# Performance work log

Measured on AMD Instinct MI355X. Metric: run time of the kernel, lower is better.

Reference implementation:

```python
import jax, jax.numpy as jnp
import numpy as np

NEG_SLOPE = 0.01  # torch nn.LeakyReLU default
B, C, H, W = 2, 128, 192, 192
K = 4            # num_cls
O = 12 * 5       # out_channels = 12 * num_mix


def _lrelu(x):
    return jnp.where(x >= 0, x, NEG_SLOPE * x)


def _conv1x1(x, w, b):
    # x: [B,K,C,H,W] (or [B,C,H,W] broadcast via K in w), w: [K,O,C], b: [K,O]
    y = jnp.einsum('bkchw,koc->bkohw', x, w)
    return y + b[None, :, :, None, None]


def setup_inputs() -> dict:
    key = jax.random.key(0)
    ks = jax.random.split(key, 12)
    s = 1.0 / np.sqrt(C)
    inp = {
        'fusion_context': jax.random.normal(ks[0], (B, C, H, W), jnp.float32),
        'seg': jax.random.randint(ks[1], (B, 1, H, W), 0, K, jnp.int64),
        'W1':  jax.random.normal(ks[2], (K, C, C), jnp.float32) * s,
        'b1':  jax.random.normal(ks[3], (K, C), jnp.float32) * s,
        'Wr1': jax.random.normal(ks[4], (K, C, C), jnp.float32) * s,
        'br1': jax.random.normal(ks[5], (K, C), jnp.float32) * s,
        'Wr2': jax.random.normal(ks[6], (K, C, C), jnp.float32) * s,
        'br2': jax.random.normal(ks[7], (K, C), jnp.float32) * s,
        'W3':  jax.random.normal(ks[8], (K, C, C), jnp.float32) * s,
        'b3':  jax.random.normal(ks[9], (K, C), jnp.float32) * s,
        'W4':  jax.random.normal(ks[10], (K, O, C), jnp.float32) * s,
        'b4':  jax.random.normal(ks[11], (K, O), jnp.float32) * s,
    }
    return inp


def reference(fusion_context, seg, W1, b1, Wr1, br1, Wr2, br2, W3, b3, W4, b4):
    x = fusion_context[:, None]                      # [B,1,C,H,W] -> broadcast over K towers
    x = jnp.broadcast_to(x, (B, K, C, H, W))
    h = _conv1x1(x, W1, b1)                          # conv1x1(ep_ch, ep_ch)
    # ResBlock_1x1: x + conv(lrelu(conv(x)))
    r = _conv1x1(_lrelu(_conv1x1(h, Wr1, br1)), Wr2, br2)
    h = h + r
    h = _conv1x1(h, W3, b3)                          # conv1x1(ep_ch, ep_ch)
    h = _lrelu(h)                                    # LeakyReLU
    conv_outs = _conv1x1(h, W4, b4)                  # [B,K,O,H,W]
    # one-hot mask-and-sum over classes
    seg2 = seg[:, 0]                                 # [B,H,W]
    one_hot = jax.nn.one_hot(seg2, K, dtype=conv_outs.dtype)  # [B,H,W,K]
    one_hot = jnp.transpose(one_hot, (0, 3, 1, 2))   # [B,K,H,W]
    out = jnp.sum(conv_outs * one_hot[:, :, None], axis=1)    # [B,O,H,W]
    return out
```

## Files before the change

### kernel.cpp

```cpp
#include <hip/hip_runtime.h>
#include <hip/hip_bf16.h>
#include <cstdint>
#include <cstddef>

constexpr int kB = 2, kC = 128, kH = 192, kW = 192, kK = 4, kO = 60;
constexpr int kHW  = kH * kW;
constexpr int NPIX = kB * kHW;
constexpr int P    = 96;
constexpr int WPB  = kHW / P;
constexpr int NWIN = NPIX / P;
constexpr int MAXG = 9;
constexpr float kSlope = 0.01f;

constexpr size_t WB_OFF    = 0;
constexpr size_t WB4_OFF   = 524288;
constexpr size_t BIAS_OFF  = 589824;
constexpr size_t BIAS4_OFF = 598016;
constexpr size_t WS_NEED   = 599040;

typedef __attribute__((ext_vector_type(8))) short bf16x8;
typedef __attribute__((ext_vector_type(4))) float f32x4;

__device__ __forceinline__ unsigned short f2bf(float f) {
  unsigned u = __float_as_uint(f);
  u += 0x7FFF + ((u >> 16) & 1);
  return (unsigned short)(u >> 16);
}
__device__ __forceinline__ float bf2f(unsigned short u) {
  return __uint_as_float(((unsigned)u) << 16);
}
__device__ __forceinline__ float load1(const float* p) { return *p; }
__device__ __forceinline__ float load1(const __hip_bfloat16* p) {
  return bf2f(*reinterpret_cast<const unsigned short*>(p));
}
__device__ __forceinline__ bf16x8 load_wfrag(const __hip_bfloat16* p) {
  return *reinterpret_cast<const bf16x8*>(p);
}
__device__ __forceinline__ bf16x8 load_wfrag(const float* p) {
  bf16x8 r;
#pragma unroll
  for (int j = 0; j < 8; ++j) r[j] = (short)f2bf(p[j]);
  return r;
}

__device__ __forceinline__ int xgrp(int r, int g) {
  return (g + r + (r >> 3)) & 15;
}

struct alignas(16) Smem {
  unsigned short Xs[P][kC];
  unsigned short Ys[P][kC];
  short ord[MAXG * 16];
  unsigned char kg[MAXG + 3];
  int cnt[kK], gpre[kK + 1], first[kK];
  int s_f32, s_onz;
};

template<typename T>
__device__ __forceinline__ void prep_body(
    const T* W1, const T* Wr1, const T* Wr2, const T* W3, const T* W4,
    const T* b1, const T* br1, const T* br2, const T* b3, const T* b4,
    char* ws, int gid) {
  unsigned short* WB  = (unsigned short*)(ws + WB_OFF);
  unsigned short* WB4 = (unsigned short*)(ws + WB4_OFF);
  float* BS  = (float*)(ws + BIAS_OFF);
  float* BS4 = (float*)(ws + BIAS4_OFF);
  if (gid < 32768) {
    const int lk = gid >> 11, fl = gid & 2047, f = fl >> 6, lane = fl & 63;
    const int l = lk >> 2, k = lk & 3;
    const int rb = f >> 3, oi = (f >> 2) & 1, ks = f & 3;
    const int quad = lane >> 4, col = lane & 15;
    const int row = rb * 32 + oi * 16 + col, c0 = ks * 32 + quad * 8;
    const T* Wsrc = (l == 0) ? W1 : (l == 1) ? Wr1 : (l == 2) ? Wr2 : W3;
    bf16x8 v = load_wfrag(Wsrc + ((size_t)(k * kC + row)) * kC + c0);
    *reinterpret_cast<bf16x8*>(WB + (size_t)lk * 16384 + f * 512 + lane * 8) = v;
  } else if (gid < 36864) {
    const int g2 = gid - 32768, k = g2 >> 10, fl = g2 & 1023, f = fl >> 6, lane = fl & 63;
    const int rb = f >> 2, ks = f & 3, quad = lane >> 4, col = lane & 15;
    const int row = rb * 16 + col, c0 = ks * 32 + quad * 8;
    bf16x8 v;
    if (row < kO) v = load_wfrag(W4 + ((size_t)(k * kO + row)) * kC + c0);
    else { for (int j = 0; j < 8; ++j) v[j] = 0; }
    *reinterpret_cast<bf16x8*>(WB4 + (size_t)k * 8192 + f * 512 + lane * 8) = v;
  } else if (gid < 38912) {
    const int g2 = gid - 36864, l = g2 >> 9, kn = g2 & 511, k = kn >> 7, n = kn & 127;
    const T* bsrc = (l == 0) ? b1 : (l == 1) ? br1 : (l == 2) ? br2 : b3;
    BS[g2] = load1(bsrc + k * kC + n);
  } else if (gid < 39168) {
    const int g2 = gid - 38912, k = g2 >> 6, n = g2 & 63;
    BS4[g2] = (n < kO) ? load1(b4 + k * kO + n) : 0.f;
  }
}

__global__ __launch_bounds__(256) void prep_kernel(
    const void* W1, const void* Wr1, const void* Wr2, const void* W3, const void* W4,
    const void* b1, const void* br1, const void* br2, const void* b3, const void* b4,
    char* ws) {
  __shared__ int s_f32;
  if (threadIdx.x == 0) s_f32 = 0;
  __syncthreads();
  const unsigned short h = ((const unsigned short*)W1)[threadIdx.x];
  if (((h >> 7) & 0xFF) >= 0x84) atomicAdd(&s_f32, 1);
  __syncthreads();
  const int gid = blockIdx.x * 256 + threadIdx.x;
  if (s_f32 > 8)
    prep_body<float>((const float*)W1, (const float*)Wr1, (const float*)Wr2,
                     (const float*)W3, (const float*)W4, (const float*)b1,
                     (const float*)br1, (const float*)br2, (const float*)b3,
                     (const float*)b4, ws, gid);
  else
    prep_body<__hip_bfloat16>((const __hip_bfloat16*)W1, (const __hip_bfloat16*)Wr1,
                              (const __hip_bfloat16*)Wr2, (const __hip_bfloat16*)W3,
                              (const __hip_bfloat16*)W4, (const __hip_bfloat16*)b1,
                              (const __hip_bfloat16*)br1, (const __hip_bfloat16*)br2,
                              (const __hip_bfloat16*)b3, (const __hip_bfloat16*)b4,
                              ws, gid);
}

template<bool SNIFFX>
__device__ __forceinline__ void prologue(const void* xraw, const void* segraw,
                                         Smem& sm, int bb, int hw0, int tid) {
  if (tid == 0) { sm.s_f32 = 0; sm.s_onz = 0; }
  if (tid < kK) sm.cnt[tid] = 0;
  __syncthreads();
  if constexpr (SNIFFX) {
    const unsigned short h = ((const unsigned short*)xraw)[tid];
    if (((h >> 7) & 0xFF) >= 0x84) atomicAdd(&sm.s_f32, 1);
  }
  if (tid < 288 && (tid & 1) && ((const unsigned*)segraw)[tid] != 0)
    atomicAdd(&sm.s_onz, 1);
  __syncthreads();
  const bool is64 = (sm.s_onz < 4);
  int myk = 0, myidx = 0;
  if (tid < P) {
    const int pg = bb * kHW + hw0 + tid;
    myk = is64 ? (int)((const long long*)segraw)[pg]
               : ((const int*)segraw)[pg];
    myidx = atomicAdd(&sm.cnt[myk], 1);
    if (myidx == 0) sm.first[myk] = tid;
  }
  __syncthreads();
  if (tid == 0) {
    int g = 0;
    for (int k = 0; k < kK; ++k) {
      sm.gpre[k] = g;
      const int gc = (sm.cnt[k] + 15) >> 4;
      for (int j = 0; j < gc; ++j) sm.kg[g + j] = (unsigned char)k;
      g += gc;
    }
    sm.gpre[kK] = g;
  }
  __syncthreads();
  if (tid < P) sm.ord[sm.gpre[myk] * 16 + myidx] = (short)tid;
  const int ngrp = sm.gpre[kK];
  if (tid < ngrp * 16) {
    const int g = tid >> 4, k2 = sm.kg[g];
    const int rel = tid - sm.gpre[k2] * 16;
    if (rel >= sm.cnt[k2])
      sm.ord[tid] = (short)(sm.first[k2] | 256);
  }
}

template<typename T>
__device__ __forceinline__ void stage(const void* xraw, unsigned short (*Xs)[kC],
                                      int bb, int hw0, int tid) {
  const T* x = (const T*)xraw;
  const size_t base = (size_t)bb * kC * kHW + hw0;
  if constexpr (sizeof(T) == 4) {
#pragma unroll
    for (int it = 0; it < 6; ++it) {
      const int flat = it * 512 + tid;
      const int c = flat / 24, j = flat - c * 24;
      const float4 v = *reinterpret_cast<const float4*>(
          (const float*)x + base + (size_t)c * kHW + j * 4);
      const float vv[4] = {v.x, v.y, v.z, v.w};
#pragma unroll
      for (int jj = 0; jj < 4; ++jj) {
        const int r = j * 4 + jj;
        Xs[r][xgrp(r, c >> 3) * 8 + (c & 7)] = f2bf(vv[jj]);
      }
    }
  } else {
#pragma unroll
    for (int it = 0; it < 3; ++it) {
      const int flat = it * 512 + tid;
      const int c = flat / 12, j = flat - c * 12;
      const bf16x8 v = *reinterpret_cast<const bf16x8*>(
          (const unsigned short*)x + base + (size_t)c * kHW + j * 8);
#pragma unroll
      for (int jj = 0; jj < 8; ++jj) {
        const int r = j * 8 + jj;
        Xs[r][xgrp(r, c >> 3) * 8 + (c & 7)] = (unsigned short)v[jj];
      }
    }
  }
}

template<typename T>
__device__ __forceinline__ void output(void* outraw, const float* Obuf,
                                       int bb, int hw0, int tid) {
  T* ob = (T*)outraw + (size_t)bb * kO * kHW + hw0;
  if constexpr (sizeof(T) == 4) {
#pragma unroll
    for (int it = 0; it < 3; ++it) {
      const int t = it * 512 + tid;
      if (t < 1440) {
        const int o = t / 24, q = t - o * 24;
        float4 v;
        v.x = Obuf[(q * 4 + 0) * 61 + o];
        v.y = Obuf[(q * 4 + 1) * 61 + o];
        v.z = Obuf[(q * 4 + 2) * 61 + o];
        v.w = Obuf[(q * 4 + 3) * 61 + o];
        *reinterpret_cast<float4*>((float*)ob + (size_t)o * kHW + q * 4) = v;
      }
    }
  } else {
#pragma unroll
    for (int it = 0; it < 6; ++it) {
      const int t = it * 512 + tid;
      if (t < 2880) {
        const int o = t / 48, q = t - o * 48;
        const unsigned u = (unsigned)f2bf(Obuf[(q * 2) * 61 + o]) |
                           ((unsigned)f2bf(Obuf[(q * 2 + 1) * 61 + o]) << 16);
        *reinterpret_cast<unsigned*>((unsigned short*)ob + (size_t)o * kHW + q * 2) = u;
      }
    }
  }
}

template<bool LRELU, bool RES>
__device__ __forceinline__ void layerP(const unsigned short (*src)[kC],
                                       unsigned short (*dst)[kC],
                                       const unsigned short* __restrict__ WBl,
                                       const float* __restrict__ BSl,
                                       const Smem& sm, int tid) {
  const int wave = tid >> 6, lane = tid & 63, quad = lane >> 4, col = lane & 15;
  const int rb = wave & 3, ch2 = wave >> 2;
  const int gs = sm.gpre[ch2 * 2], ge = sm.gpre[ch2 * 2 + 2];
  int curk = -1;
  bf16x8 a[2][4];
  float bs[2][4];
  for (int g = gs; g < ge; ++g) {
    const int k = sm.kg[g];
    if (k != curk) {
      curk = k;
      const unsigned short* wk = WBl + (size_t)k * 16384 + lane * 8;
#pragma unroll
      for (int oi = 0; oi < 2; ++oi) {
#pragma unroll
        for (int ks = 0; ks < 4; ++ks)
          a[oi][ks] = *reinterpret_cast<const bf16x8*>(wk + (((rb * 2 + oi) * 4 + ks) << 9));
        const float4 bv = *reinterpret_cast<const float4*>(
            BSl + k * kC + rb * 32 + oi * 16 + quad * 4);
        bs[oi][0] = bv.x; bs[oi][1] = bv.y; bs[oi][2] = bv.z; bs[oi][3] = bv.w;
      }
    }
    const int ov  = sm.ord[g * 16 + col];
    const int row = ov & 255;
    bf16x8 bfr[4];
#pragma unroll
    for (int ks = 0; ks < 4; ++ks)
      bfr[ks] = *reinterpret_cast<const bf16x8*>(&src[row][xgrp(row, ks * 4 + quad) * 8]);
#pragma unroll
    for (int oi = 0; oi < 2; ++oi) {
      f32x4 acc = {0.f, 0.f, 0.f, 0.f};
#pragma unroll
      for (int ks = 0; ks < 4; ++ks)
        acc = __builtin_amdgcn_mfma_f32_16x16x32_bf16(a[oi][ks], bfr[ks], acc, 0, 0, 0);
      if (ov < 256) {
        const int nb = rb * 32 + oi * 16 + quad * 4;
        unsigned short* dp = &dst[row][xgrp(row, nb >> 3) * 8 + (nb & 7)];
        float v[4];
#pragma unroll
        for (int r = 0; r < 4; ++r) {
          float t = acc[r] + bs[oi][r];
          if constexpr (LRELU) t = (t >= 0.f) ? t : kSlope * t;
          v[r] = t;
        }
        if constexpr (RES) {
          const short4 rv = *reinterpret_cast<const short4*>(dp);
          v[0] += bf2f((unsigned short)rv.x);
          v[1] += bf2f((unsigned short)rv.y);
          v[2] += bf2f((unsigned short)rv.z);
          v[3] += bf2f((unsigned short)rv.w);
        }
        short4 pk;
        pk.x = (short)f2bf(v[0]); pk.y = (short)f2bf(v[1]);
        pk.z = (short)f2bf(v[2]); pk.w = (short)f2bf(v[3]);
        *reinterpret_cast<short4*>(dp) = pk;
      }
    }
  }
}

__device__ __forceinline__ void layer5P(const unsigned short (*src)[kC],
                                        float* __restrict__ Obuf,
                                        const unsigned short* __restrict__ WB4,
                                        const float* __restrict__ BS4,
                                        const Smem& sm, int tid) {
  const int wave = tid >> 6, lane = tid & 63, quad = lane >> 4, col = lane & 15;
  const int rb = wave & 3, ch2 = wave >> 2;
  const int gs = sm.gpre[ch2 * 2], ge = sm.gpre[ch2 * 2 + 2];
  int curk = -1;
  bf16x8 a[4];
  float bs[4];
  for (int g = gs; g < ge; ++g) {
    const int k = sm.kg[g];
    if (k != curk) {
      curk = k;
      const unsigned short* wk = WB4 + (size_t)k * 8192 + lane * 8;
#pragma unroll
      for (int ks = 0; ks < 4; ++ks)
        a[ks] = *reinterpret_cast<const bf16x8*>(wk + ((rb * 4 + ks) << 9));
      const float4 bv = *reinterpret_cast<const float4*>(BS4 + k * 64 + rb * 16 + quad * 4);
      bs[0] = bv.x; bs[1] = bv.y; bs[2] = bv.z; bs[3] = bv.w;
    }
    const int ov  = sm.ord[g * 16 + col];
    const int row = ov & 255;
    bf16x8 bfr[4];
#pragma unroll
    for (int ks = 0; ks < 4; ++ks)
      bfr[ks] = *reinterpret_cast<const bf16x8*>(&src[row][xgrp(row, ks * 4 + quad) * 8]);
    f32x4 acc = {0.f, 0.f, 0.f, 0.f};
#pragma unroll
    for (int ks = 0; ks < 4; ++ks)
      acc = __builtin_amdgcn_mfma_f32_16x16x32_bf16(a[ks], bfr[ks], acc, 0, 0, 0);
    if (ov < 256) {
#pragma unroll
      for (int r = 0; r < 4; ++r) {
        const int n = rb * 16 + quad * 4 + r;
        if (n < kO) Obuf[row * 61 + n] = acc[r] + bs[r];
      }
    }
  }
}

__global__ __launch_bounds__(512) void fused_main(const void* xraw, const void* segraw,
                                                  void* outraw,
                                                  const char* __restrict__ ws) {
  __shared__ Smem sm;
  const int tid = threadIdx.x, wi = blockIdx.x;
  const int bb = wi / WPB, hw0 = (wi - bb * WPB) * P;
  prologue<true>(xraw, segraw, sm, bb, hw0, tid);
  const bool isf32 = (sm.s_f32 > 16);
  if (isf32) stage<float>(xraw, sm.Xs, bb, hw0, tid);
  else       stage<__hip_bfloat16>(xraw, sm.Xs, bb, hw0, tid);
  __syncthreads();

  const unsigned short* WB  = (const unsigned short*)(ws + WB_OFF);
  const unsigned short* WB4 = (const unsigned short*)(ws + WB4_OFF);
  const float* BS  = (const float*)(ws + BIAS_OFF);
  const float* BS4 = (const float*)(ws + BIAS4_OFF);

  layerP<false, false>(sm.Xs, sm.Ys, WB,              BS,        sm, tid); __syncthreads();
  layerP<true,  false>(sm.Ys, sm.Xs, WB + 4 * 16384,  BS + 512,  sm, tid); __syncthreads();
  layerP<false, true >(sm.Xs, sm.Ys, WB + 8 * 16384,  BS + 1024, sm, tid); __syncthreads();
  layerP<true,  false>(sm.Ys, sm.Xs, WB + 12 * 16384, BS + 1536, sm, tid); __syncthreads();
  float* Obuf = (float*)sm.Ys;
  layer5P(sm.Xs, Obuf, WB4, BS4, sm, tid);     __syncthreads();

  if (isf32) output<float>(outraw, Obuf, bb, hw0, tid);
  else       output<__hip_bfloat16>(outraw, Obuf, bb, hw0, tid);
}

template<typename T, bool LRELU, bool RES>
__device__ __forceinline__ void layerF(const unsigned short (*src)[kC],
                                       unsigned short (*dst)[kC],
                                       const T* __restrict__ W,
                                       const T* __restrict__ bia,
                                       const Smem& sm, int tid) {
  const int wave = tid >> 6, lane = tid & 63, quad = lane >> 4, col = lane & 15;
  const int rb = wave & 3, ch2 = wave >> 2;
  const int gs = sm.gpre[ch2 * 2], ge = sm.gpre[ch2 * 2 + 2];
  int curk = -1;
  bf16x8 a[2][4];
  float bs[2][4];
  for (int g = gs; g < ge; ++g) {
    const int k = sm.kg[g];
    if (k != curk) {
      curk = k;
      const T* Wk = W + (size_t)k * kC * kC;
      const T* bk = bia + (size_t)k * kC;
#pragma unroll
      for (int oi = 0; oi < 2; ++oi) {
        const int ra = rb * 32 + oi * 16 + col;
#pragma unroll
        for (int ks = 0; ks < 4; ++ks)
          a[oi][ks] = load_wfrag(Wk + (size_t)ra * kC + ks * 32 + quad * 8);
#pragma unroll
        for (int r = 0; r < 4; ++r)
          bs[oi][r] = load1(bk + rb * 32 + oi * 16 + quad * 4 + r);
      }
    }
    const int ov  = sm.ord[g * 16 + col];
    const int row = ov & 255;
    bf16x8 bfr[4];
#pragma unroll
    for (int ks = 0; ks < 4; ++ks)
      bfr[ks] = *reinterpret_cast<const bf16x8*>(&src[row][xgrp(row, ks * 4 + quad) * 8]);
#pragma unroll
    for (int oi = 0; oi < 2; ++oi) {
      f32x4 acc = {0.f, 0.f, 0.f, 0.f};
#pragma unroll
      for (int ks = 0; ks < 4; ++ks)
        acc = __builtin_amdgcn_mfma_f32_16x16x32_bf16(a[oi][ks], bfr[ks], acc, 0, 0, 0);
      if (ov < 256) {
        const int nb = rb * 32 + oi * 16 + quad * 4;
        unsigned short* dp = &dst[row][xgrp(row, nb >> 3) * 8 + (nb & 7)];
        float v[4];
#pragma unroll
        for (int r = 0; r < 4; ++r) {
          float t = acc[r] + bs[oi][r];
          if constexpr (LRELU) t = (t >= 0.f) ? t : kSlope * t;
          v[r] = t;
        }
        if constexpr (RES) {
          const short4 rv = *reinterpret_cast<const short4*>(dp);
          v[0] += bf2f((unsigned short)rv.x);
          v[1] += bf2f((unsigned short)rv.y);
          v[2] += bf2f((unsigned short)rv.z);
          v[3] += bf2f((unsigned short)rv.w);
        }
        short4 pk;
        pk.x = (short)f2bf(v[0]); pk.y = (short)f2bf(v[1]);
        pk.z = (short)f2bf(v[2]); pk.w = (short)f2bf(v[3]);
        *reinterpret_cast<short4*>(dp) = pk;
      }
    }
  }
}

template<typename T>
__device__ __forceinline__ void layer5F(const unsigned short (*src)[kC],
                                        float* __restrict__ Obuf,
                                        const T* __restrict__ W4,
                                        const T* __restrict__ b4,
                                        const Smem& sm, int tid) {
  const int wave = tid >> 6, lane = tid & 63, quad = lane >> 4, col = lane & 15;
  const int rb = wave & 3, ch2 = wave >> 2;
  const int gs = sm.gpre[ch2 * 2], ge = sm.gpre[ch2 * 2 + 2];
  int curk = -1;
  bf16x8 a[4];
  float bs[4];
  for (int g = gs; g < ge; ++g) {
    const int k = sm.kg[g];
    if (k != curk) {
      curk = k;
      const T* Wk = W4 + (size_t)k * kO * kC;
      const T* bk = b4 + (size_t)k * kO;
      const int ra = min(rb * 16 + col, kO - 1);
#pragma unroll
      for (int ks = 0; ks < 4; ++ks)
        a[ks] = load_wfrag(Wk + (size_t)ra * kC + ks * 32 + quad * 8);
#pragma unroll
      for (int r = 0; r < 4; ++r) {
        const int n = rb * 16 + quad * 4 + r;
        bs[r] = (n < kO) ? load1(bk + n) : 0.f;
      }
    }
    const int ov  = sm.ord[g * 16 + col];
    const int row = ov & 255;
    bf16x8 bfr[4];
#pragma unroll
    for (int ks = 0; ks < 4; ++ks)
      bfr[ks] = *reinterpret_cast<const bf16x8*>(&src[row][xgrp(row, ks * 4 + quad) * 8]);
    f32x4 acc = {0.f, 0.f, 0.f, 0.f};
#pragma unroll
    for (int ks = 0; ks < 4; ++ks)
      acc = __builtin_amdgcn_mfma_f32_16x16x32_bf16(a[ks], bfr[ks], acc, 0, 0, 0);
    if (ov < 256) {
#pragma unroll
      for (int r = 0; r < 4; ++r) {
        const int n = rb * 16 + quad * 4 + r;
        if (n < kO) Obuf[row * 61 + n] = acc[r] + bs[r];
      }
    }
  }
}

template<typename T>
__device__ __forceinline__ void run_fall(
    const void* xraw, void* outraw,
    const void* W1, const void* b1, const void* Wr1, const void* br1,
    const void* Wr2, const void* br2, const void* W3, const void* b3,
    const void* W4, const void* b4,
    Smem& sm, int bb, int hw0, int tid) {
  stage<T>(xraw, sm.Xs, bb, hw0, tid);
  __syncthreads();
  layerF<T, false, false>(sm.Xs, sm.Ys, (const T*)W1,  (const T*)b1,  sm, tid); __syncthreads();
  layerF<T, true,  false>(sm.Ys, sm.Xs, (const T*)Wr1, (const T*)br1, sm, tid); __syncthreads();
  layerF<T, false, true >(sm.Xs, sm.Ys, (const T*)Wr2, (const T*)br2, sm, tid); __syncthreads();
  layerF<T, true,  false>(sm.Ys, sm.Xs, (const T*)W3,  (const T*)b3,  sm, tid); __syncthreads();
  float* Obuf = (float*)sm.Ys;
  layer5F<T>(sm.Xs, Obuf, (const T*)W4, (const T*)b4, sm, tid);
  __syncthreads();
  output<T>(outraw, Obuf, bb, hw0, tid);
}

__global__ __launch_bounds__(512) void fused_fallback(
    const void* xraw, const void* segraw,
    const void* W1, const void* b1, const void* Wr1, const void* br1,
    const void* Wr2, const void* br2, const void* W3, const void* b3,
    const void* W4, const void* b4, void* outraw) {
  __shared__ Smem sm;
  const int tid = threadIdx.x, wi = blockIdx.x;
  const int bb = wi / WPB, hw0 = (wi - bb * WPB) * P;
  prologue<true>(xraw, segraw, sm, bb, hw0, tid);
  if (sm.s_f32 > 16)
    run_fall<float>(xraw, outraw, W1, b1, Wr1, br1, Wr2, br2, W3, b3, W4, b4,
                    sm, bb, hw0, tid);
  else
    run_fall<__hip_bfloat16>(xraw, outraw, W1, b1, Wr1, br1, Wr2, br2, W3, b3, W4, b4,
                             sm, bb, hw0, tid);
}

extern "C" void kernel_launch(void* const* d_in, const int* in_sizes, int n_in,
                              void* d_out, int out_size, void* d_ws, size_t ws_size,
                              hipStream_t stream) {
  (void)in_sizes; (void)n_in; (void)out_size;
  const int prep = (d_ws != nullptr && ws_size >= WS_NEED) ? 1 : 0;
  if (prep) {
    prep_kernel<<<153, 256, 0, stream>>>(
        d_in[2], d_in[4], d_in[6], d_in[8], d_in[10],
        d_in[3], d_in[5], d_in[7], d_in[9], d_in[11], (char*)d_ws);
    fused_main<<<NWIN, 512, 0, stream>>>(d_in[0], d_in[1], d_out, (const char*)d_ws);
  } else {
    fused_fallback<<<NWIN, 512, 0, stream>>>(
        d_in[0], d_in[1], d_in[2], d_in[3], d_in[4], d_in[5], d_in[6], d_in[7],
        d_in[8], d_in[9], d_in[10], d_in[11], d_out);
  }
}
```

Baseline: 132.4 us.

## Run whole 5-layer MLP per wave on a 16-pixel group, dropping block barriers

Replaces the block-cooperative layer-by-layer scheme, in which waves split output rows and sync after each layer, with a per-wave pipeline. Each wave owns one 16-pixel class group and runs all five layers on it through a private 16-row LDS scratch, keeping the residual in registers. This removes the inter-layer __syncthreads and the Ys buffer. In exchange every wave now streams the full weight matrix for each layer from global/L2 (8x more weight loads per wave), and load balance depends on the group count (up to 9 groups over 8 waves, so one wave may do two groups).

```diff
diff --git a/kernel.cpp b/kernel.cpp
--- a/kernel.cpp
+++ b/kernel.cpp
@@ -47,6 +47,14 @@
   return (g + r + (r >> 3)) & 15;
 }
 
+struct alignas(16) Smem2 {
+  unsigned short Xs[P][kC];
+  unsigned short Scr[8 * 16 * kC];
+  short ord[MAXG * 16];
+  unsigned char kg[MAXG + 3];
+  int cnt[kK], gpre[kK + 1], first[kK];
+  int s_f32, s_onz;
+};
 struct alignas(16) Smem {
   unsigned short Xs[P][kC];
   unsigned short Ys[P][kC];
@@ -117,9 +125,9 @@
                               ws, gid);
 }
 
-template<bool SNIFFX>
+template<bool SNIFFX, typename SM>
 __device__ __forceinline__ void prologue(const void* xraw, const void* segraw,
-                                         Smem& sm, int bb, int hw0, int tid) {
+                                         SM& sm, int bb, int hw0, int tid) {
   if (tid == 0) { sm.s_f32 = 0; sm.s_onz = 0; }
   if (tid < kK) sm.cnt[tid] = 0;
   __syncthreads();
@@ -228,117 +236,112 @@
   }
 }
 
-template<bool LRELU, bool RES>
-__device__ __forceinline__ void layerP(const unsigned short (*src)[kC],
-                                       unsigned short (*dst)[kC],
-                                       const unsigned short* __restrict__ WBl,
-                                       const float* __restrict__ BSl,
-                                       const Smem& sm, int tid) {
-  const int wave = tid >> 6, lane = tid & 63, quad = lane >> 4, col = lane & 15;
-  const int rb = wave & 3, ch2 = wave >> 2;
-  const int gs = sm.gpre[ch2 * 2], ge = sm.gpre[ch2 * 2 + 2];
-  int curk = -1;
-  bf16x8 a[2][4];
-  float bs[2][4];
-  for (int g = gs; g < ge; ++g) {
-    const int k = sm.kg[g];
-    if (k != curk) {
-      curk = k;
-      const unsigned short* wk = WBl + (size_t)k * 16384 + lane * 8;
-#pragma unroll
-      for (int oi = 0; oi < 2; ++oi) {
-#pragma unroll
-        for (int ks = 0; ks < 4; ++ks)
-          a[oi][ks] = *reinterpret_cast<const bf16x8*>(wk + (((rb * 2 + oi) * 4 + ks) << 9));
-        const float4 bv = *reinterpret_cast<const float4*>(
-            BSl + k * kC + rb * 32 + oi * 16 + quad * 4);
-        bs[oi][0] = bv.x; bs[oi][1] = bv.y; bs[oi][2] = bv.z; bs[oi][3] = bv.w;
-      }
-    }
-    const int ov  = sm.ord[g * 16 + col];
-    const int row = ov & 255;
-    bf16x8 bfr[4];
-#pragma unroll
-    for (int ks = 0; ks < 4; ++ks)
-      bfr[ks] = *reinterpret_cast<const bf16x8*>(&src[row][xgrp(row, ks * 4 + quad) * 8]);
-#pragma unroll
-    for (int oi = 0; oi < 2; ++oi) {
-      f32x4 acc = {0.f, 0.f, 0.f, 0.f};
-#pragma unroll
-      for (int ks = 0; ks < 4; ++ks)
-        acc = __builtin_amdgcn_mfma_f32_16x16x32_bf16(a[oi][ks], bfr[ks], acc, 0, 0, 0);
-      if (ov < 256) {
-        const int nb = rb * 32 + oi * 16 + quad * 4;
-        unsigned short* dp = &dst[row][xgrp(row, nb >> 3) * 8 + (nb & 7)];
-        float v[4];
-#pragma unroll
-        for (int r = 0; r < 4; ++r) {
-          float t = acc[r] + bs[oi][r];
-          if constexpr (LRELU) t = (t >= 0.f) ? t : kSlope * t;
-          v[r] = t;
-        }
-        if constexpr (RES) {
-          const short4 rv = *reinterpret_cast<const short4*>(dp);
-          v[0] += bf2f((unsigned short)rv.x);
-          v[1] += bf2f((unsigned short)rv.y);
-          v[2] += bf2f((unsigned short)rv.z);
-          v[3] += bf2f((unsigned short)rv.w);
-        }
-        short4 pk;
-        pk.x = (short)f2bf(v[0]); pk.y = (short)f2bf(v[1]);
-        pk.z = (short)f2bf(v[2]); pk.w = (short)f2bf(v[3]);
-        *reinterpret_cast<short4*>(dp) = pk;
-      }
-    }
-  }
-}
-
-__device__ __forceinline__ void layer5P(const unsigned short (*src)[kC],
-                                        float* __restrict__ Obuf,
-                                        const unsigned short* __restrict__ WB4,
-                                        const float* __restrict__ BS4,
-                                        const Smem& sm, int tid) {
-  const int wave = tid >> 6, lane = tid & 63, quad = lane >> 4, col = lane & 15;
-  const int rb = wave & 3, ch2 = wave >> 2;
-  const int gs = sm.gpre[ch2 * 2], ge = sm.gpre[ch2 * 2 + 2];
-  int curk = -1;
-  bf16x8 a[4];
-  float bs[4];
-  for (int g = gs; g < ge; ++g) {
-    const int k = sm.kg[g];
-    if (k != curk) {
-      curk = k;
-      const unsigned short* wk = WB4 + (size_t)k * 8192 + lane * 8;
-#pragma unroll
-      for (int ks = 0; ks < 4; ++ks)
-        a[ks] = *reinterpret_cast<const bf16x8*>(wk + ((rb * 4 + ks) << 9));
-      const float4 bv = *reinterpret_cast<const float4*>(BS4 + k * 64 + rb * 16 + quad * 4);
-      bs[0] = bv.x; bs[1] = bv.y; bs[2] = bv.z; bs[3] = bv.w;
-    }
-    const int ov  = sm.ord[g * 16 + col];
-    const int row = ov & 255;
-    bf16x8 bfr[4];
-#pragma unroll
-    for (int ks = 0; ks < 4; ++ks)
-      bfr[ks] = *reinterpret_cast<const bf16x8*>(&src[row][xgrp(row, ks * 4 + quad) * 8]);
+template<bool LRELU, bool RES, bool SAVE>
+__device__ __forceinline__ void wave_layer(
+    const unsigned short* __restrict__ wbase,
+    const float* __restrict__ bbase,
+    bf16x8 (&b)[4], uint2 (&resid)[8],
+    unsigned short* scr, int c, int q) {
+#pragma unroll
+  for (int t = 0; t < 8; ++t) {
+    const bf16x8 a0 = *reinterpret_cast<const bf16x8*>(wbase + ((t * 4 + 0) << 9));
+    const bf16x8 a1 = *reinterpret_cast<const bf16x8*>(wbase + ((t * 4 + 1) << 9));
+    const bf16x8 a2 = *reinterpret_cast<const bf16x8*>(wbase + ((t * 4 + 2) << 9));
+    const bf16x8 a3 = *reinterpret_cast<const bf16x8*>(wbase + ((t * 4 + 3) << 9));
     f32x4 acc = {0.f, 0.f, 0.f, 0.f};
-#pragma unroll
-    for (int ks = 0; ks < 4; ++ks)
-      acc = __builtin_amdgcn_mfma_f32_16x16x32_bf16(a[ks], bfr[ks], acc, 0, 0, 0);
-    if (ov < 256) {
-#pragma unroll
-      for (int r = 0; r < 4; ++r) {
-        const int n = rb * 16 + quad * 4 + r;
-        if (n < kO) Obuf[row * 61 + n] = acc[r] + bs[r];
-      }
-    }
-  }
+    acc = __builtin_amdgcn_mfma_f32_16x16x32_bf16(a0, b[0], acc, 0, 0, 0);
+    acc = __builtin_amdgcn_mfma_f32_16x16x32_bf16(a1, b[1], acc, 0, 0, 0);
+    acc = __builtin_amdgcn_mfma_f32_16x16x32_bf16(a2, b[2], acc, 0, 0, 0);
+    acc = __builtin_amdgcn_mfma_f32_16x16x32_bf16(a3, b[3], acc, 0, 0, 0);
+    const float4 bv = *reinterpret_cast<const float4*>(bbase + t * 16);
+    float v0 = acc[0] + bv.x, v1 = acc[1] + bv.y;
+    float v2 = acc[2] + bv.z, v3 = acc[3] + bv.w;
+    if constexpr (RES) {
+      v0 += bf2f((unsigned short)(resid[t].x & 0xFFFFu));
+      v1 += bf2f((unsigned short)(resid[t].x >> 16));
+      v2 += bf2f((unsigned short)(resid[t].y & 0xFFFFu));
+      v3 += bf2f((unsigned short)(resid[t].y >> 16));
+    }
+    if constexpr (LRELU) {
+      v0 = (v0 >= 0.f) ? v0 : kSlope * v0;
+      v1 = (v1 >= 0.f) ? v1 : kSlope * v1;
+      v2 = (v2 >= 0.f) ? v2 : kSlope * v2;
+      v3 = (v3 >= 0.f) ? v3 : kSlope * v3;
+    }
+    uint2 pk;
+    pk.x = (unsigned)f2bf(v0) | ((unsigned)f2bf(v1) << 16);
+    pk.y = (unsigned)f2bf(v2) | ((unsigned)f2bf(v3) << 16);
+    if constexpr (SAVE) resid[t] = pk;
+    *reinterpret_cast<uint2*>(
+        scr + c * kC + xgrp(c, 2 * t + (q >> 1)) * 8 + 4 * (q & 1)) = pk;
+  }
+#pragma unroll
+  for (int s = 0; s < 4; ++s)
+    b[s] = *reinterpret_cast<const bf16x8*>(scr + c * kC + xgrp(c, s * 4 + q) * 8);
+}
+
+__device__ __forceinline__ void wave_layer5(
+    const unsigned short* __restrict__ wbase,
+    const float* __restrict__ bbase,
+    const bf16x8 (&b)[4], f32x4 (&out)[4]) {
+#pragma unroll
+  for (int t = 0; t < 4; ++t) {
+    const bf16x8 a0 = *reinterpret_cast<const bf16x8*>(wbase + ((t * 4 + 0) << 9));
+    const bf16x8 a1 = *reinterpret_cast<const bf16x8*>(wbase + ((t * 4 + 1) << 9));
+    const bf16x8 a2 = *reinterpret_cast<const bf16x8*>(wbase + ((t * 4 + 2) << 9));
+    const bf16x8 a3 = *reinterpret_cast<const bf16x8*>(wbase + ((t * 4 + 3) << 9));
+    f32x4 acc = {0.f, 0.f, 0.f, 0.f};
+    acc = __builtin_amdgcn_mfma_f32_16x16x32_bf16(a0, b[0], acc, 0, 0, 0);
+    acc = __builtin_amdgcn_mfma_f32_16x16x32_bf16(a1, b[1], acc, 0, 0, 0);
+    acc = __builtin_amdgcn_mfma_f32_16x16x32_bf16(a2, b[2], acc, 0, 0, 0);
+    acc = __builtin_amdgcn_mfma_f32_16x16x32_bf16(a3, b[3], acc, 0, 0, 0);
+    const float4 bv = *reinterpret_cast<const float4*>(bbase + t * 16);
+    out[t][0] = acc[0] + bv.x;
+    out[t][1] = acc[1] + bv.y;
+    out[t][2] = acc[2] + bv.z;
+    out[t][3] = acc[3] + bv.w;
+  }
+}
+
+__device__ __forceinline__ void run_group(
+    const Smem2& sm, const char* __restrict__ ws, int g, int c, int q, int lane,
+    unsigned short* scr, f32x4 (&out)[4], int& rowOut, bool& valid) {
+  const int k = sm.kg[g];
+  const int ov = sm.ord[g * 16 + c];
+  const int row = ov & 255;
+  rowOut = row;
+  valid = (ov < 256);
+  bf16x8 b[4];
+#pragma unroll
+  for (int s = 0; s < 4; ++s)
+    b[s] = *reinterpret_cast<const bf16x8*>(&sm.Xs[row][xgrp(row, s * 4 + q) * 8]);
+  uint2 resid[8];
+  const unsigned short* WB = (const unsigned short*)(ws + WB_OFF) + lane * 8;
+  const float* BS = (const float*)(ws + BIAS_OFF) + q * 4;
+  wave_layer<false, false, true >(WB + (size_t)(0 * 4 + k) * 16384, BS + (0 * 4 + k) * kC, b, resid, scr, c, q);
+  wave_layer<true,  false, false>(WB + (size_t)(1 * 4 + k) * 16384, BS + (1 * 4 + k) * kC, b, resid, scr, c, q);
+  wave_layer<false, true,  false>(WB + (size_t)(2 * 4 + k) * 16384, BS + (2 * 4 + k) * kC, b, resid, scr, c, q);
+  wave_layer<true,  false, false>(WB + (size_t)(3 * 4 + k) * 16384, BS + (3 * 4 + k) * kC, b, resid, scr, c, q);
+  const unsigned short* WB4 = (const unsigned short*)(ws + WB4_OFF) + (size_t)k * 8192 + lane * 8;
+  const float* BS4 = (const float*)(ws + BIAS4_OFF) + k * 64 + q * 4;
+  wave_layer5(WB4, BS4, b, out);
+}
+
+__device__ __forceinline__ void obuf_write(float* Obuf, const f32x4 (&out)[4],
+                                           int row, int q) {
+#pragma unroll
+  for (int t = 0; t < 4; ++t)
+#pragma unroll
+    for (int r = 0; r < 4; ++r) {
+      const int n = t * 16 + q * 4 + r;
+      if (n < kO) Obuf[row * 61 + n] = out[t][r];
+    }
 }
 
 __global__ __launch_bounds__(512) void fused_main(const void* xraw, const void* segraw,
                                                   void* outraw,
                                                   const char* __restrict__ ws) {
-  __shared__ Smem sm;
+  __shared__ Smem2 sm;
   const int tid = threadIdx.x, wi = blockIdx.x;
   const int bb = wi / WPB, hw0 = (wi - bb * WPB) * P;
   prologue<true>(xraw, segraw, sm, bb, hw0, tid);
@@ -347,18 +350,19 @@
   else       stage<__hip_bfloat16>(xraw, sm.Xs, bb, hw0, tid);
   __syncthreads();
 
-  const unsigned short* WB  = (const unsigned short*)(ws + WB_OFF);
-  const unsigned short* WB4 = (const unsigned short*)(ws + WB4_OFF);
-  const float* BS  = (const float*)(ws + BIAS_OFF);
-  const float* BS4 = (const float*)(ws + BIAS4_OFF);
-
-  layerP<false, false>(sm.Xs, sm.Ys, WB,              BS,        sm, tid); __syncthreads();
-  layerP<true,  false>(sm.Ys, sm.Xs, WB + 4 * 16384,  BS + 512,  sm, tid); __syncthreads();
-  layerP<false, true >(sm.Xs, sm.Ys, WB + 8 * 16384,  BS + 1024, sm, tid); __syncthreads();
-  layerP<true,  false>(sm.Ys, sm.Xs, WB + 12 * 16384, BS + 1536, sm, tid); __syncthreads();
-  float* Obuf = (float*)sm.Ys;
-  layer5P(sm.Xs, Obuf, WB4, BS4, sm, tid);     __syncthreads();
-
+  const int wave = tid >> 6, lane = tid & 63, q = lane >> 4, c = lane & 15;
+  unsigned short* scr = sm.Scr + wave * 16 * kC;
+  const int ngrp = sm.gpre[kK];
+  f32x4 outA[4], outB[4];
+  int rowA = 0, rowB = 0;
+  bool vA = false, vB = false;
+  if (wave < ngrp)     run_group(sm, ws, wave,     c, q, lane, scr, outA, rowA, vA);
+  if (wave + 8 < ngrp) run_group(sm, ws, wave + 8, c, q, lane, scr, outB, rowB, vB);
+  __syncthreads();
+  float* Obuf = reinterpret_cast<float*>(sm.Xs);
+  if (vA) obuf_write(Obuf, outA, rowA, q);
+  if (vB) obuf_write(Obuf, outB, rowB, q);
+  __syncthreads();
   if (isf32) output<float>(outraw, Obuf, bb, hw0, tid);
   else       output<__hip_bfloat16>(outraw, Obuf, bb, hw0, tid);
 }
```

New measurement: 146.4 us. +10.6%, slower.
